# Kernel optimization log

Hardware: AMD Instinct MI355X
Metric: run time of the kernel (lower is better)

Reference implementation:

```python
import jax, jax.numpy as jnp
import numpy as np

D_MODEL = 1024
NUM_HEADS = 16
D_K = D_MODEL // NUM_HEADS


def setup_inputs() -> dict:
    key = jax.random.key(0)
    ks = jax.random.split(key, 12)
    B, S = 2, 2048
    s = 1.0 / np.sqrt(D_MODEL)
    inp = {
        "query": jax.random.normal(ks[0], (B, S, D_MODEL), jnp.float32),
        "key": jax.random.normal(ks[1], (B, S, D_MODEL), jnp.float32),
        "value": jax.random.normal(ks[2], (B, S, D_MODEL), jnp.float32),
        "Wq": jax.random.normal(ks[3], (D_MODEL, D_MODEL), jnp.float32) * s,
        "bq": jax.random.normal(ks[4], (D_MODEL,), jnp.float32) * s,
        "Wk": jax.random.normal(ks[5], (D_MODEL, D_MODEL), jnp.float32) * s,
        "bk": jax.random.normal(ks[6], (D_MODEL,), jnp.float32) * s,
        "Wv": jax.random.normal(ks[7], (D_MODEL, D_MODEL), jnp.float32) * s,
        "bv": jax.random.normal(ks[8], (D_MODEL,), jnp.float32) * s,
        "Wo": jax.random.normal(ks[9], (D_MODEL, D_MODEL), jnp.float32) * s,
        "bo": jax.random.normal(ks[10], (D_MODEL,), jnp.float32) * s,
    }
    return inp


def _split_heads(x):
    B, S, _ = x.shape
    return x.reshape(B, S, NUM_HEADS, D_K).transpose(0, 2, 1, 3)  # [B,H,S,Dk]


def reference(query, key, value, Wq, bq, Wk, bk, Wv, bv, Wo, bo):
    # Linear projections (torch Linear: x @ W.T + b)
    Q = _split_heads(query @ Wq.T + bq)
    K = _split_heads(key @ Wk.T + bk)
    V = _split_heads(value @ Wv.T + bv)
    scale = 1.0 / jnp.sqrt(jnp.asarray(D_K, Q.dtype))
    scores = jnp.einsum('bhqd,bhkd->bhqk', Q, K) * scale  # [B,H,S,S]
    attn = jax.nn.softmax(scores, axis=-1)
    # dropout is identity in eval mode
    x = jnp.einsum('bhqk,bhkd->bhqd', attn, V)
    B, H, S, Dk = x.shape
    x = x.transpose(0, 2, 1, 3).reshape(B, S, H * Dk)
    return x @ Wo.T + bo
```

## Files before the change

kernel.cpp:

```cpp
#include <hip/hip_runtime.h>
#include <hip/hip_bf16.h>

typedef __bf16 bf16;
typedef __attribute__((ext_vector_type(4))) __bf16 bf16x4;
typedef __attribute__((ext_vector_type(8))) __bf16 bf16x8;
typedef __attribute__((ext_vector_type(4))) float f32x4;
typedef __attribute__((ext_vector_type(16))) float f32x16;
typedef unsigned int u32;

#define D_MODEL 1024
#define NHEADS 16
#define DK 64
#define BATCH 2
#define SEQ 2048
#define NTOK (BATCH * SEQ)

#define QSCALE 0.18033688011112042f

__device__ __forceinline__ u32 cvtpk_bf16(float lo, float hi) {
  u32 r;
  asm("v_cvt_pk_bf16_f32 %0, %1, %2" : "=v"(r) : "v"(lo), "v"(hi));
  return r;
}
__device__ __forceinline__ void plswap(u32& a, u32& b) {
  asm("v_permlane32_swap_b32 %0, %1" : "+v"(a), "+v"(b));
}
__device__ __forceinline__ float fast_exp2(float x) {
#if __has_builtin(__builtin_amdgcn_exp2f)
  return __builtin_amdgcn_exp2f(x);
#else
  return exp2f(x);
#endif
}
__device__ __forceinline__ float xhalf_add(float x) {
  return x + __shfl_xor(x, 32);
}

__device__ __forceinline__ int frag_off_q(int s, int d) {
  return ((s >> 5) << 11) + ((d >> 4) << 9) + ((((d >> 3) & 1) * 32 + (s & 31)) << 3) + (d & 7);
}
__device__ __forceinline__ int frag_off_k(int s, int d) {
  return ((s >> 6) << 12) + ((((s >> 5) & 1) * 4 + (d >> 4)) << 9) +
         ((((d >> 3) & 1) * 32 + (s & 31)) << 3) + (d & 7);
}
__device__ __forceinline__ int frag_off_v(int s, int d) {
  return ((s >> 6) << 12) + (((d >> 5) * 4 + ((s >> 4) & 3)) << 9) +
         ((((s >> 3) & 1) * 32 + (d & 31)) << 3) + (s & 7);
}

__global__ __launch_bounds__(256) void cvt3_kernel(
    const float* __restrict__ s0, const float* __restrict__ s1, const float* __restrict__ s2,
    bf16* __restrict__ d0, bf16* __restrict__ d1, bf16* __restrict__ d2, int n4) {
  int i = blockIdx.x * blockDim.x + threadIdx.x;
  if (i >= n4) return;
  const float* s = blockIdx.y == 0 ? s0 : blockIdx.y == 1 ? s1 : s2;
  bf16* d = blockIdx.y == 0 ? d0 : blockIdx.y == 1 ? d1 : d2;
  float4 v = reinterpret_cast<const float4*>(s)[i];
  bf16x4 o;
  o[0] = (bf16)v.x; o[1] = (bf16)v.y; o[2] = (bf16)v.z; o[3] = (bf16)v.w;
  reinterpret_cast<bf16x4*>(d)[i] = o;
}

__global__ __launch_bounds__(256) void cvt4_kernel(
    const float* __restrict__ s0, const float* __restrict__ s1,
    const float* __restrict__ s2, const float* __restrict__ s3,
    bf16* __restrict__ d0, bf16* __restrict__ d1, bf16* __restrict__ d2, bf16* __restrict__ d3,
    int n4) {
  int i = blockIdx.x * blockDim.x + threadIdx.x;
  if (i >= n4) return;
  const float* s = blockIdx.y == 0 ? s0 : blockIdx.y == 1 ? s1 : blockIdx.y == 2 ? s2 : s3;
  bf16* d = blockIdx.y == 0 ? d0 : blockIdx.y == 1 ? d1 : blockIdx.y == 2 ? d2 : d3;
  float4 v = reinterpret_cast<const float4*>(s)[i];
  bf16x4 o;
  o[0] = (bf16)v.x; o[1] = (bf16)v.y; o[2] = (bf16)v.z; o[3] = (bf16)v.w;
  reinterpret_cast<bf16x4*>(d)[i] = o;
}

#define ASYNC_COPY16(gptr, lptr)                                                \
  __builtin_amdgcn_global_load_lds(                                             \
      (__attribute__((address_space(1))) void*)(gptr),                          \
      (__attribute__((address_space(3))) void*)(lptr), 16, 0, 0)

#define BK 64

struct ProjArgs {
  const bf16* A[3];
  const bf16* W[3];
  const float* bias[3];
  bf16* out[3];
};

__global__ __launch_bounds__(256) void gemm_proj(ProjArgs pa, int K) {
  __shared__ bf16 smem[2][128][BK];
  bf16 (*As)[BK] = smem[0];
  bf16 (*Bs)[BK] = smem[1];
  const int z = blockIdx.z;
  const bf16* A = pa.A[z];
  const bf16* Bw = pa.W[z];
  const int m0 = blockIdx.x * 128;
  const int n0 = blockIdx.y * 128;

  const int t = threadIdx.x;
  const int wave = t >> 6;
  const int lane = t & 63;
  const int wr = (wave >> 1) * 64;
  const int wc = (wave & 1) * 64;
  const int srow = lane >> 3;
  const int scol = ((lane & 7) ^ srow) * 8;
  const int fr = lane & 15;
  const int fk = (lane >> 4) * 8;
  const int fx = (fr & 7) * 8;

  f32x4 acc[4][4] = {};

  for (int k0 = 0; k0 < K; k0 += BK) {
#pragma unroll
    for (int j = 0; j < 4; j++) {
      const int r = wave * 32 + j * 8;
      ASYNC_COPY16(&A[(size_t)(m0 + r + srow) * K + k0 + scol], &As[r][0]);
      ASYNC_COPY16(&Bw[(size_t)(n0 + r + srow) * K + k0 + scol], &Bs[r][0]);
    }
    __syncthreads();

    bf16x8 af[4][2], bfr[4][2];
#pragma unroll
    for (int m = 0; m < 4; m++) {
      af[m][0] = *reinterpret_cast<const bf16x8*>(&As[wr + m * 16 + fr][(fk) ^ fx]);
      af[m][1] = *reinterpret_cast<const bf16x8*>(&As[wr + m * 16 + fr][(32 + fk) ^ fx]);
    }
#pragma unroll
    for (int n = 0; n < 4; n++) {
      bfr[n][0] = *reinterpret_cast<const bf16x8*>(&Bs[wc + n * 16 + fr][(fk) ^ fx]);
      bfr[n][1] = *reinterpret_cast<const bf16x8*>(&Bs[wc + n * 16 + fr][(32 + fk) ^ fx]);
    }
#pragma unroll
    for (int kk = 0; kk < 2; kk++)
#pragma unroll
      for (int m = 0; m < 4; m++)
#pragma unroll
        for (int n = 0; n < 4; n++)
          acc[m][n] = __builtin_amdgcn_mfma_f32_16x16x32_bf16(af[m][kk], bfr[n][kk], acc[m][n], 0, 0, 0);
    __syncthreads();
  }

  bf16* cbuf = &smem[0][0][0];
  const float scale = (z == 0) ? QSCALE : 1.0f;
  const float* bias = pa.bias[z];
#pragma unroll
  for (int m = 0; m < 4; m++) {
#pragma unroll
    for (int n = 0; n < 4; n++) {
      const int col = n0 + wc + n * 16 + fr;
      const float bv = bias[col];
      const int d = col & (DK - 1);
      const int h_loc = (col >> 6) & 1;
#pragma unroll
      for (int j = 0; j < 4; j++) {
        const int rl = wr + m * 16 + (lane >> 4) * 4 + j;
        const float v = (acc[m][n][j] + bv) * scale;
        int inner;
        if (z == 0)      inner = frag_off_q(rl, d);
        else if (z == 1) inner = frag_off_k(rl, d);
        else             inner = frag_off_v(rl, d);
        cbuf[h_loc * 8192 + inner] = (bf16)v;
      }
    }
  }
  __syncthreads();

  {
    const int bblk = m0 >> 11;
    const int ms = m0 & (SEQ - 1);
    const int h_loc = t >> 7;
    const int tl = t & 127;
    const int h = (n0 >> 6) + h_loc;
    bf16* outp = pa.out[z] + ((size_t)(bblk * NHEADS + h)) * SEQ * DK + (size_t)ms * 64;
#pragma unroll
    for (int c = 0; c < 8; c++) {
      const int off_e = (tl + c * 128) * 8;
      *reinterpret_cast<bf16x8*>(&outp[off_e]) =
          *reinterpret_cast<const bf16x8*>(&cbuf[h_loc * 8192 + off_e]);
    }
  }
}

__global__ __launch_bounds__(256) void gemm_out(
    const bf16* __restrict__ A, const bf16* __restrict__ Bw,
    const float* __restrict__ bias, float* __restrict__ out, int K) {
  __shared__ bf16 As[128][BK];
  __shared__ bf16 Bs[64][BK];
  const int m0 = blockIdx.x * 128;
  const int n0 = blockIdx.y * 64;

  const int t = threadIdx.x;
  const int wave = t >> 6;
  const int lane = t & 63;
  const int wr = (wave >> 1) * 64;
  const int wc = (wave & 1) * 32;
  const int srow = lane >> 3;
  const int scol = ((lane & 7) ^ srow) * 8;
  const int fr = lane & 15;
  const int fk = (lane >> 4) * 8;
  const int fx = (fr & 7) * 8;

  f32x4 acc[4][2] = {};

  for (int k0 = 0; k0 < K; k0 += BK) {
#pragma unroll
    for (int j = 0; j < 4; j++) {
      const int r = wave * 32 + j * 8;
      ASYNC_COPY16(&A[(size_t)(m0 + r + srow) * K + k0 + scol], &As[r][0]);
    }
#pragma unroll
    for (int j = 0; j < 2; j++) {
      const int r = wave * 16 + j * 8;
      ASYNC_COPY16(&Bw[(size_t)(n0 + r + srow) * K + k0 + scol], &Bs[r][0]);
    }
    __syncthreads();

    bf16x8 af[4][2], bfr[2][2];
#pragma unroll
    for (int m = 0; m < 4; m++) {
      af[m][0] = *reinterpret_cast<const bf16x8*>(&As[wr + m * 16 + fr][(fk) ^ fx]);
      af[m][1] = *reinterpret_cast<const bf16x8*>(&As[wr + m * 16 + fr][(32 + fk) ^ fx]);
    }
#pragma unroll
    for (int n = 0; n < 2; n++) {
      bfr[n][0] = *reinterpret_cast<const bf16x8*>(&Bs[wc + n * 16 + fr][(fk) ^ fx]);
      bfr[n][1] = *reinterpret_cast<const bf16x8*>(&Bs[wc + n * 16 + fr][(32 + fk) ^ fx]);
    }
#pragma unroll
    for (int kk = 0; kk < 2; kk++)
#pragma unroll
      for (int m = 0; m < 4; m++)
#pragma unroll
        for (int n = 0; n < 2; n++)
          acc[m][n] = __builtin_amdgcn_mfma_f32_16x16x32_bf16(af[m][kk], bfr[n][kk], acc[m][n], 0, 0, 0);
    __syncthreads();
  }

#pragma unroll
  for (int m = 0; m < 4; m++) {
#pragma unroll
    for (int n = 0; n < 2; n++) {
      const int col = n0 + wc + n * 16 + fr;
      const float bv = bias[col];
#pragma unroll
      for (int j = 0; j < 4; j++) {
        const int row = m0 + wr + m * 16 + (lane >> 4) * 4 + j;
        out[(size_t)row * D_MODEL + col] = acc[m][n][j] + bv;
      }
    }
  }
}

#define QBLK 32
#define KVBLK 32
#define NT (SEQ / KVBLK)

__global__ __launch_bounds__(256, 2) void attn_kernel(
    const bf16* __restrict__ Qf,
    const bf16* __restrict__ Kf,
    const bf16* __restrict__ Vf,
    bf16* __restrict__ X) {
  const int lane = threadIdx.x & 63;
  const int wave = threadIdx.x >> 6;

  const int i = blockIdx.x;
  const int xcd = i & 7;
  const int slot = i >> 3;
  const int hgrp = slot >> 4;
  const int xq = slot & 15;
  const int bh = xcd + 8 * hgrp;
  const int bb = bh >> 4, hh = bh & (NHEADS - 1);
  const int q0 = xq * (QBLK * 4) + wave * QBLK;
  const int row = lane & 31, hi = lane >> 5;

  const bf16* Qp = Qf + (size_t)bh * SEQ * DK + (size_t)q0 * DK;
  const bf16* Kp = Kf + (size_t)bh * SEQ * DK;
  const bf16* Vp = Vf + (size_t)bh * SEQ * DK;

  bf16x8 qf[4];
#pragma unroll
  for (int kd = 0; kd < 4; kd++)
    qf[kd] = *reinterpret_cast<const bf16x8*>(&Qp[kd * 512 + lane * 8]);

  f32x16 ot0, ot1, fz;
#pragma unroll
  for (int r = 0; r < 16; r++) { ot0[r] = 0.f; ot1[r] = 0.f; fz[r] = 0.f; }
  float l_run = 0.f;

  bf16x8 ka[4], kb[4];

#define LOADK32(dst, tt)                                                        \
  {                                                                             \
    const bf16* kbase_ = Kp + (size_t)(tt) * 2048 + lane * 8;                   \
    _Pragma("unroll") for (int kd = 0; kd < 4; kd++)                            \
        dst[kd] = *reinterpret_cast<const bf16x8*>(&kbase_[kd * 512]);          \
  }

  LOADK32(ka, 0)
  LOADK32(kb, 1)
  f32x16 sa, sb;
  __builtin_amdgcn_s_setprio(1);
  sa = __builtin_amdgcn_mfma_f32_32x32x16_bf16(ka[0], qf[0], fz, 0, 0, 0);
#pragma unroll
  for (int kd = 1; kd < 4; kd++)
    sa = __builtin_amdgcn_mfma_f32_32x32x16_bf16(ka[kd], qf[kd], sa, 0, 0, 0);
  __builtin_amdgcn_s_setprio(0);

  auto pipe = [&](f32x16& SC, f32x16& SN, bf16x8 (&KN)[4], bf16x8 (&KL)[4], int tc) {
    __builtin_amdgcn_s_setprio(1);
    SN = __builtin_amdgcn_mfma_f32_32x32x16_bf16(KN[0], qf[0], fz, 0, 0, 0);
#pragma unroll
    for (int kd = 1; kd < 4; kd++)
      SN = __builtin_amdgcn_mfma_f32_32x32x16_bf16(KN[kd], qf[kd], SN, 0, 0, 0);
    __builtin_amdgcn_s_setprio(0);

    LOADK32(KL, (tc + 2) & (NT - 1))

    bf16x8 vf[2][2];
    {
      const bf16* vbase_ = Vp + (size_t)(tc >> 1) * 4096 + lane * 8;
      const int so = (tc & 1) * 2;
#pragma unroll
      for (int dh = 0; dh < 2; dh++)
#pragma unroll
        for (int ks = 0; ks < 2; ks++)
          vf[dh][ks] = *reinterpret_cast<const bf16x8*>(
              &vbase_[(dh * 4 + so + ks) * 512]);
    }

    float p[16];
#pragma unroll
    for (int r = 0; r < 16; r++) p[r] = fast_exp2(SC[r]);
    float a8[8];
#pragma unroll
    for (int r = 0; r < 8; r++) a8[r] = p[r] + p[r + 8];
#pragma unroll
    for (int r = 0; r < 4; r++) a8[r] += a8[r + 4];
    l_run += (a8[0] + a8[1]) + (a8[2] + a8[3]);

    u32 c[8];
#pragma unroll
    for (int i2 = 0; i2 < 8; i2++) c[i2] = cvtpk_bf16(p[2 * i2], p[2 * i2 + 1]);
    plswap(c[0], c[2]);   plswap(c[1], c[3]);
    plswap(c[4], c[6]);   plswap(c[5], c[7]);
    bf16x8 pbv[2];
#pragma unroll
    for (int ks = 0; ks < 2; ks++) {
      union { u32 u[4]; bf16x8 v; } pk;
      pk.u[0] = c[ks * 4 + 0]; pk.u[1] = c[ks * 4 + 1];
      pk.u[2] = c[ks * 4 + 2]; pk.u[3] = c[ks * 4 + 3];
      pbv[ks] = pk.v;
    }

    __builtin_amdgcn_s_setprio(1);
    ot0 = __builtin_amdgcn_mfma_f32_32x32x16_bf16(vf[0][0], pbv[0], ot0, 0, 0, 0);
    ot0 = __builtin_amdgcn_mfma_f32_32x32x16_bf16(vf[0][1], pbv[1], ot0, 0, 0, 0);
    ot1 = __builtin_amdgcn_mfma_f32_32x32x16_bf16(vf[1][0], pbv[0], ot1, 0, 0, 0);
    ot1 = __builtin_amdgcn_mfma_f32_32x32x16_bf16(vf[1][1], pbv[1], ot1, 0, 0, 0);
    __builtin_amdgcn_s_setprio(0);
  };

  for (int t = 0; t < NT; t += 2) {
    pipe(sa, sb, kb, ka, t);
    pipe(sb, sa, ka, kb, t + 1);
  }

  l_run = xhalf_add(l_run);

  const float inv = 1.0f / l_run;
  bf16* Xp = X + ((size_t)bb * SEQ + q0 + row) * D_MODEL + hh * DK;
#pragma unroll
  for (int g = 0; g < 4; g++) {
    bf16x4 w0, w1;
#pragma unroll
    for (int j = 0; j < 4; j++) {
      w0[j] = (bf16)(ot0[g * 4 + j] * inv);
      w1[j] = (bf16)(ot1[g * 4 + j] * inv);
    }
    *reinterpret_cast<bf16x4*>(&Xp[g * 8 + hi * 4]) = w0;
    *reinterpret_cast<bf16x4*>(&Xp[32 + g * 8 + hi * 4]) = w1;
  }
}

extern "C" void kernel_launch(void* const* d_in, const int* in_sizes, int n_in,
                              void* d_out, int out_size, void* d_ws, size_t ws_size,
                              hipStream_t stream) {
  const float* q  = (const float*)d_in[0];
  const float* k  = (const float*)d_in[1];
  const float* v  = (const float*)d_in[2];
  const float* Wq = (const float*)d_in[3];
  const float* bq = (const float*)d_in[4];
  const float* Wk = (const float*)d_in[5];
  const float* bk = (const float*)d_in[6];
  const float* Wv = (const float*)d_in[7];
  const float* bv = (const float*)d_in[8];
  const float* Wo = (const float*)d_in[9];
  const float* bo = (const float*)d_in[10];

  char* ws = (char*)d_ws;
  size_t off = 0;
  auto alloc = [&](size_t bytes) -> void* {
    void* p = ws + off;
    off += (bytes + 255) & ~(size_t)255;
    return p;
  };
  const size_t ACT = (size_t)NTOK * D_MODEL;
  const size_t WEL = (size_t)D_MODEL * D_MODEL;

  bf16* Xq  = (bf16*)alloc(ACT * 2);
  bf16* Xk  = (bf16*)alloc(ACT * 2);
  bf16* Xv  = (bf16*)alloc(ACT * 2);
  bf16* Wqb = (bf16*)alloc(WEL * 2);
  bf16* Wkb = (bf16*)alloc(WEL * 2);
  bf16* Wvb = (bf16*)alloc(WEL * 2);
  bf16* Wob = (bf16*)alloc(WEL * 2);
  bf16* Qfb = (bf16*)alloc(ACT * 2);
  bf16* Kfb = (bf16*)alloc(ACT * 2);
  bf16* Vfb = (bf16*)alloc(ACT * 2);
  bf16* Xa  = (bf16*)alloc(ACT * 2);

  {
    int n4 = (int)(ACT / 4);
    cvt3_kernel<<<dim3((n4 + 255) / 256, 3), dim3(256), 0, stream>>>(q, k, v, Xq, Xk, Xv, n4);
  }
  {
    int n4 = (int)(WEL / 4);
    cvt4_kernel<<<dim3((n4 + 255) / 256, 4), dim3(256), 0, stream>>>(
        Wq, Wk, Wv, Wo, Wqb, Wkb, Wvb, Wob, n4);
  }

  ProjArgs pa;
  pa.A[0] = Xq;  pa.A[1] = Xk;  pa.A[2] = Xv;
  pa.W[0] = Wqb; pa.W[1] = Wkb; pa.W[2] = Wvb;
  pa.bias[0] = bq; pa.bias[1] = bk; pa.bias[2] = bv;
  pa.out[0] = Qfb; pa.out[1] = Kfb; pa.out[2] = Vfb;
  gemm_proj<<<dim3(NTOK / 128, D_MODEL / 128, 3), dim3(256), 0, stream>>>(pa, D_MODEL);

  attn_kernel<<<dim3(512), dim3(256), 0, stream>>>(Qfb, Kfb, Vfb, Xa);

  gemm_out<<<dim3(NTOK / 128, D_MODEL / 64), dim3(256), 0, stream>>>(
      Xa, Wob, bo, (float*)d_out, D_MODEL);
}
```

Measured before the change: 131.7 us.

## Double-buffer projection and output GEMM tiles with async LDS loads

Both the QKV projection GEMM and the output GEMM now use two LDS buffers with a K-step of 32 instead of one buffer with a K-step of 64. The next tile's global-to-LDS async copy is issued before the current tile is consumed by MFMA, and only one barrier runs per step instead of two. The goal is to hide global load latency behind matrix math. In exchange there are twice as many loop iterations, and the XOR swizzle on the LDS layout is removed, so fragment reads along rows with a 64-byte stride may hit LDS bank conflicts.

```diff
diff --git a/kernel.cpp b/kernel.cpp
--- a/kernel.cpp
+++ b/kernel.cpp
@@ -81,7 +81,8 @@
       (__attribute__((address_space(1))) void*)(gptr),                          \
       (__attribute__((address_space(3))) void*)(lptr), 16, 0, 0)
 
-#define BK 64
+#define BK 32
+#define NSTEP (D_MODEL / BK)
 
 struct ProjArgs {
   const bf16* A[3];
@@ -91,9 +92,7 @@
 };
 
 __global__ __launch_bounds__(256) void gemm_proj(ProjArgs pa, int K) {
-  __shared__ bf16 smem[2][128][BK];
-  bf16 (*As)[BK] = smem[0];
-  bf16 (*Bs)[BK] = smem[1];
+  __shared__ bf16 smem[2][2][128][BK];
   const int z = blockIdx.z;
   const bf16* A = pa.A[z];
   const bf16* Bw = pa.W[z];
@@ -105,45 +104,50 @@
   const int lane = t & 63;
   const int wr = (wave >> 1) * 64;
   const int wc = (wave & 1) * 64;
-  const int srow = lane >> 3;
-  const int scol = ((lane & 7) ^ srow) * 8;
+  const int r4 = lane >> 2;
+  const int c8 = (lane & 3) * 8;
   const int fr = lane & 15;
   const int fk = (lane >> 4) * 8;
-  const int fx = (fr & 7) * 8;
 
   f32x4 acc[4][4] = {};
 
-  for (int k0 = 0; k0 < K; k0 += BK) {
-#pragma unroll
-    for (int j = 0; j < 4; j++) {
-      const int r = wave * 32 + j * 8;
-      ASYNC_COPY16(&A[(size_t)(m0 + r + srow) * K + k0 + scol], &As[r][0]);
-      ASYNC_COPY16(&Bw[(size_t)(n0 + r + srow) * K + k0 + scol], &Bs[r][0]);
-    }
+#define STAGE_PROJ(buf, kk0)                                                    \
+  {                                                                             \
+    ASYNC_COPY16(&A[(size_t)(m0 + wave * 16 + r4) * K + (kk0) + c8],            \
+                 &smem[buf][0][wave * 16][0]);                                  \
+    ASYNC_COPY16(&A[(size_t)(m0 + 64 + wave * 16 + r4) * K + (kk0) + c8],       \
+                 &smem[buf][0][64 + wave * 16][0]);                             \
+    ASYNC_COPY16(&Bw[(size_t)(n0 + wave * 16 + r4) * K + (kk0) + c8],           \
+                 &smem[buf][1][wave * 16][0]);                                  \
+    ASYNC_COPY16(&Bw[(size_t)(n0 + 64 + wave * 16 + r4) * K + (kk0) + c8],      \
+                 &smem[buf][1][64 + wave * 16][0]);                             \
+  }
+
+  STAGE_PROJ(0, 0)
+  __syncthreads();
+
+  int cur = 0;
+  for (int s = 0; s < NSTEP; s++) {
+    if (s + 1 < NSTEP) STAGE_PROJ(cur ^ 1, (s + 1) * BK)
+
+    bf16x8 af[4], bfr[4];
+#pragma unroll
+    for (int m = 0; m < 4; m++)
+      af[m] = *reinterpret_cast<const bf16x8*>(&smem[cur][0][wr + m * 16 + fr][fk]);
+#pragma unroll
+    for (int n = 0; n < 4; n++)
+      bfr[n] = *reinterpret_cast<const bf16x8*>(&smem[cur][1][wc + n * 16 + fr][fk]);
+#pragma unroll
+    for (int m = 0; m < 4; m++)
+#pragma unroll
+      for (int n = 0; n < 4; n++)
+        acc[m][n] = __builtin_amdgcn_mfma_f32_16x16x32_bf16(af[m], bfr[n], acc[m][n], 0, 0, 0);
+
     __syncthreads();
-
-    bf16x8 af[4][2], bfr[4][2];
-#pragma unroll
-    for (int m = 0; m < 4; m++) {
-      af[m][0] = *reinterpret_cast<const bf16x8*>(&As[wr + m * 16 + fr][(fk) ^ fx]);
-      af[m][1] = *reinterpret_cast<const bf16x8*>(&As[wr + m * 16 + fr][(32 + fk) ^ fx]);
-    }
-#pragma unroll
-    for (int n = 0; n < 4; n++) {
-      bfr[n][0] = *reinterpret_cast<const bf16x8*>(&Bs[wc + n * 16 + fr][(fk) ^ fx]);
-      bfr[n][1] = *reinterpret_cast<const bf16x8*>(&Bs[wc + n * 16 + fr][(32 + fk) ^ fx]);
-    }
-#pragma unroll
-    for (int kk = 0; kk < 2; kk++)
-#pragma unroll
-      for (int m = 0; m < 4; m++)
-#pragma unroll
-        for (int n = 0; n < 4; n++)
-          acc[m][n] = __builtin_amdgcn_mfma_f32_16x16x32_bf16(af[m][kk], bfr[n][kk], acc[m][n], 0, 0, 0);
-    __syncthreads();
-  }
-
-  bf16* cbuf = &smem[0][0][0];
+    cur ^= 1;
+  }
+
+  bf16* cbuf = &smem[0][0][0][0];
   const float scale = (z == 0) ? QSCALE : 1.0f;
   const float* bias = pa.bias[z];
 #pragma unroll
@@ -187,8 +191,8 @@
 __global__ __launch_bounds__(256) void gemm_out(
     const bf16* __restrict__ A, const bf16* __restrict__ Bw,
     const float* __restrict__ bias, float* __restrict__ out, int K) {
-  __shared__ bf16 As[128][BK];
-  __shared__ bf16 Bs[64][BK];
+  __shared__ bf16 AsO[2][128][BK];
+  __shared__ bf16 BsO[2][64][BK];
   const int m0 = blockIdx.x * 128;
   const int n0 = blockIdx.y * 64;
 
@@ -197,46 +201,45 @@
   const int lane = t & 63;
   const int wr = (wave >> 1) * 64;
   const int wc = (wave & 1) * 32;
-  const int srow = lane >> 3;
-  const int scol = ((lane & 7) ^ srow) * 8;
+  const int r4 = lane >> 2;
+  const int c8 = (lane & 3) * 8;
   const int fr = lane & 15;
   const int fk = (lane >> 4) * 8;
-  const int fx = (fr & 7) * 8;
 
   f32x4 acc[4][2] = {};
 
-  for (int k0 = 0; k0 < K; k0 += BK) {
-#pragma unroll
-    for (int j = 0; j < 4; j++) {
-      const int r = wave * 32 + j * 8;
-      ASYNC_COPY16(&A[(size_t)(m0 + r + srow) * K + k0 + scol], &As[r][0]);
-    }
-#pragma unroll
-    for (int j = 0; j < 2; j++) {
-      const int r = wave * 16 + j * 8;
-      ASYNC_COPY16(&Bw[(size_t)(n0 + r + srow) * K + k0 + scol], &Bs[r][0]);
-    }
+#define STAGE_OUT(buf, kk0)                                                     \
+  {                                                                             \
+    ASYNC_COPY16(&A[(size_t)(m0 + wave * 16 + r4) * K + (kk0) + c8],            \
+                 &AsO[buf][wave * 16][0]);                                      \
+    ASYNC_COPY16(&A[(size_t)(m0 + 64 + wave * 16 + r4) * K + (kk0) + c8],       \
+                 &AsO[buf][64 + wave * 16][0]);                                 \
+    ASYNC_COPY16(&Bw[(size_t)(n0 + wave * 16 + r4) * K + (kk0) + c8],           \
+                 &BsO[buf][wave * 16][0]);                                      \
+  }
+
+  STAGE_OUT(0, 0)
+  __syncthreads();
+
+  int cur = 0;
+  for (int s = 0; s < NSTEP; s++) {
+    if (s + 1 < NSTEP) STAGE_OUT(cur ^ 1, (s + 1) * BK)
+
+    bf16x8 af[4], bfr[2];
+#pragma unroll
+    for (int m = 0; m < 4; m++)
+      af[m] = *reinterpret_cast<const bf16x8*>(&AsO[cur][wr + m * 16 + fr][fk]);
+#pragma unroll
+    for (int n = 0; n < 2; n++)
+      bfr[n] = *reinterpret_cast<const bf16x8*>(&BsO[cur][wc + n * 16 + fr][fk]);
+#pragma unroll
+    for (int m = 0; m < 4; m++)
+#pragma unroll
+      for (int n = 0; n < 2; n++)
+        acc[m][n] = __builtin_amdgcn_mfma_f32_16x16x32_bf16(af[m], bfr[n], acc[m][n], 0, 0, 0);
+
     __syncthreads();
-
-    bf16x8 af[4][2], bfr[2][2];
-#pragma unroll
-    for (int m = 0; m < 4; m++) {
-      af[m][0] = *reinterpret_cast<const bf16x8*>(&As[wr + m * 16 + fr][(fk) ^ fx]);
-      af[m][1] = *reinterpret_cast<const bf16x8*>(&As[wr + m * 16 + fr][(32 + fk) ^ fx]);
-    }
-#pragma unroll
-    for (int n = 0; n < 2; n++) {
-      bfr[n][0] = *reinterpret_cast<const bf16x8*>(&Bs[wc + n * 16 + fr][(fk) ^ fx]);
-      bfr[n][1] = *reinterpret_cast<const bf16x8*>(&Bs[wc + n * 16 + fr][(32 + fk) ^ fx]);
-    }
-#pragma unroll
-    for (int kk = 0; kk < 2; kk++)
-#pragma unroll
-      for (int m = 0; m < 4; m++)
-#pragma unroll
-        for (int n = 0; n < 2; n++)
-          acc[m][n] = __builtin_amdgcn_mfma_f32_16x16x32_bf16(af[m][kk], bfr[n][kk], acc[m][n], 0, 0, 0);
-    __syncthreads();
+    cur ^= 1;
   }
 
 #pragma unroll
```

New measurement: 125.4 us. -4.8%, faster.
